# Performance work log

Hardware: AMD Instinct MI355X
Metric: run time of the kernel (lower is better)

Reference implementation:

```python
import jax, jax.numpy as jnp
import numpy as np

DIM = 64; N_C = 2000; N_P = 1500; N_ATOMS = 40; L_PROT = 512
N_FP = 10000; N_WORD = 8000; DIM_D = 1024; DIM_P = 1024
L_GNN = 3; L_CNN = 3; L_GCN = 2; WIN = 5; B = 4096


def setup_inputs() -> dict:
    key = jax.random.key(0)
    ks = jax.random.split(key, 32)
    g = lambda i, shape, s=0.05: jax.random.normal(ks[i], shape, dtype=jnp.float32) * s
    inp = {}
    inp["idx_c"] = jax.random.randint(ks[0], (B,), 0, N_C)
    inp["idx_p"] = jax.random.randint(ks[1], (B,), 0, N_P)
    inp["compounds"] = jax.random.randint(ks[2], (N_C, N_ATOMS), 0, N_FP)
    inp["proteins"] = jax.random.randint(ks[3], (N_P, L_PROT), 0, N_WORD)
    a = (jax.random.uniform(ks[4], (N_C, N_ATOMS, N_ATOMS)) < 0.1).astype(jnp.float32)
    inp["adjacencies"] = jnp.clip(a + jnp.swapaxes(a, 1, 2) + jnp.eye(N_ATOMS), 0.0, 1.0)
    ac = (jax.random.uniform(ks[5], (N_C, N_C)) < 0.005).astype(jnp.float32)
    inp["A_c"] = jnp.clip(ac + ac.T + jnp.eye(N_C), 0.0, 1.0) / 20.0
    ap = (jax.random.uniform(ks[6], (N_P, N_P)) < 0.005).astype(jnp.float32)
    inp["A_p"] = jnp.clip(ap + ap.T + jnp.eye(N_P), 0.0, 1.0) / 20.0
    inp["embed_fp"] = g(7, (N_FP, DIM), 1.0)
    inp["embed_word"] = g(8, (N_WORD, DIM), 1.0)
    inp["Xs_c"] = g(9, (N_C, DIM), 1.0)
    inp["Xs_p"] = g(10, (N_P, DIM), 1.0)
    inp["drug_feat"] = g(11, (N_C, DIM_D), 1.0)
    inp["protein_feat"] = g(12, (N_P, DIM_P), 1.0)
    inp["W_gnn"] = g(13, (L_GNN, DIM, DIM)); inp["b_gnn"] = jnp.zeros((L_GNN, DIM), jnp.float32)
    inp["K_cnn"] = g(14, (L_CNN, 2 * WIN + 1, 2 * WIN + 1)); inp["b_cnn"] = jnp.zeros((L_CNN,), jnp.float32)
    inp["W_gcn_d"] = g(15, (L_GCN, DIM, DIM)); inp["b_gcn_d"] = jnp.zeros((L_GCN, DIM), jnp.float32)
    inp["W_gcn_p"] = g(16, (L_GCN, DIM, DIM)); inp["b_gcn_p"] = jnp.zeros((L_GCN, DIM), jnp.float32)
    inp["Wd1"] = g(17, (DIM_D, 2 * DIM)); inp["bd1"] = jnp.zeros((2 * DIM,), jnp.float32)
    inp["Wd2"] = g(18, (2 * DIM, DIM)); inp["bd2"] = jnp.zeros((DIM,), jnp.float32)
    inp["Wd3"] = g(19, (DIM, DIM)); inp["bd3"] = jnp.zeros((DIM,), jnp.float32)
    inp["Wp1"] = g(20, (DIM_P, 2 * DIM)); inp["bp1"] = jnp.zeros((2 * DIM,), jnp.float32)
    inp["Wp2"] = g(21, (2 * DIM, DIM)); inp["bp2"] = jnp.zeros((DIM,), jnp.float32)
    inp["Wp3"] = g(22, (DIM, DIM)); inp["bp3"] = jnp.zeros((DIM,), jnp.float32)
    inp["Wo1"] = g(23, (6 * DIM, 4 * DIM)); inp["bo1"] = jnp.zeros((4 * DIM,), jnp.float32)
    inp["Wo2"] = g(24, (4 * DIM, 4 * DIM)); inp["bo2"] = jnp.zeros((4 * DIM,), jnp.float32)
    inp["Wo3"] = g(25, (4 * DIM, 4 * DIM)); inp["bo3"] = jnp.zeros((4 * DIM,), jnp.float32)
    inp["W_int"] = g(26, (4 * DIM, 2)); inp["b_int"] = jnp.zeros((2,), jnp.float32)
    return inp


def reference(idx_c, idx_p, compounds, proteins, adjacencies, A_c, A_p,
              embed_fp, embed_word, Xs_c, Xs_p, drug_feat, protein_feat,
              W_gnn, b_gnn, K_cnn, b_cnn, W_gcn_d, b_gcn_d, W_gcn_p, b_gcn_p,
              Wd1, bd1, Wd2, bd2, Wd3, bd3, Wp1, bp1, Wp2, bp2, Wp3, bp3,
              Wo1, bo1, Wo2, bo2, Wo3, bo3, W_int, b_int):
    # ---- intrinsic compound embedding: batched GNN over all compounds.
    # (travInvolve's BFS selects a superset of idx_c; computing all rows is
    #  output-equivalent since only Xs_c_int[idx_c] is consumed.)
    xs = embed_fp[compounds]                                  # [N_c, A, d]
    for i in range(L_GNN):
        hs = jax.nn.relu(jnp.einsum('nad,de->nae', xs, W_gnn[i]) + b_gnn[i])
        xs = xs + jnp.einsum('nab,nbd->nad', adjacencies, hs)
    comp_int = jnp.mean(xs, axis=1)                           # [N_c, d]

    # ---- intrinsic protein embedding: batched single-channel 2D CNN (SAME pad)
    x = embed_word[proteins][:, None]                         # [N_p, 1, L, d]
    for i in range(L_CNN):
        x = jax.nn.relu(jax.lax.conv_general_dilated(
            x, K_cnn[i][None, None], (1, 1), [(WIN, WIN), (WIN, WIN)]) + b_cnn[i])
    prot_int = jnp.mean(x[:, 0], axis=1)                      # mean over length -> [N_p, d]

    # ---- relational GCN diffusion over global adjacency
    Xc = Xs_c
    for i in range(L_GCN):
        Xc = jax.nn.relu((A_c @ Xc) @ W_gcn_d[i] + b_gcn_d[i])
    Xp = Xs_p
    for i in range(L_GCN):
        Xp = jax.nn.relu((A_p @ Xp) @ W_gcn_p[i] + b_gcn_p[i])

    # ---- annotation MLPs
    fd = jax.nn.relu(drug_feat[idx_c] @ Wd1 + bd1)
    fd = jax.nn.relu(fd @ Wd2 + bd2)
    fd = jax.nn.relu(fd @ Wd3 + bd3)
    fp = jax.nn.relu(protein_feat[idx_p] @ Wp1 + bp1)
    fp = jax.nn.relu(fp @ Wp2 + bp2)
    fp = jax.nn.relu(fp @ Wp3 + bp3)

    cat = jnp.concatenate([comp_int[idx_c], Xc[idx_c], fd,
                           prot_int[idx_p], Xp[idx_p], fp], axis=1)  # [B, 6d]
    h = jax.nn.relu(cat @ Wo1 + bo1)
    h = jax.nn.relu(h @ Wo2 + bo2)
    h = jax.nn.relu(h @ Wo3 + bo3)
    return jax.nn.sigmoid(h @ W_int + b_int)                  # [B, 2]
```

## Files before the change

### kernel.cpp

```cpp
#include <hip/hip_runtime.h>
#include <math.h>

#define NC 2000
#define NP 1500
#define NA 40
#define LP 512
#define BSZ 4096
#define NW 8000
#define KPC 2048
#define KPP 1536

typedef _Float16 half8_t __attribute__((ext_vector_type(8)));
typedef _Float16 half4_t __attribute__((ext_vector_type(4)));
typedef float f32x4 __attribute__((ext_vector_type(4)));

__device__ __forceinline__ int swz_off(int row, int half_col)
{
    int b = half_col >> 3;
    return row * 128 + (((b & 8) | ((b ^ row) & 7)) << 3) + (half_col & 7);
}

__global__ void prep_all(
    const float* __restrict__ K_cnn, _Float16* __restrict__ wtab,
    const float* __restrict__ ew, _Float16* __restrict__ ehp,
    const float* __restrict__ df, const float* __restrict__ pf,
    const float* __restrict__ wd1, const float* __restrict__ wd2, const float* __restrict__ wd3,
    const float* __restrict__ wp1, const float* __restrict__ wp2, const float* __restrict__ wp3,
    const float* __restrict__ wo1, const float* __restrict__ wo2, const float* __restrict__ wo3,
    _Float16* __restrict__ dfh, _Float16* __restrict__ pfh,
    _Float16* __restrict__ wd1t, _Float16* __restrict__ wd2t, _Float16* __restrict__ wd3t,
    _Float16* __restrict__ wp1t, _Float16* __restrict__ wp2t, _Float16* __restrict__ wp3t,
    _Float16* __restrict__ wo1t, _Float16* __restrict__ wo2t, _Float16* __restrict__ wo3t,
    const float* __restrict__ wgnn, _Float16* __restrict__ wgt,
    const float* __restrict__ Ac, const float* __restrict__ Ap,
    const float* __restrict__ Xc, const float* __restrict__ Xp,
    _Float16* __restrict__ Ahc, _Float16* __restrict__ Ahp,
    _Float16* __restrict__ Xtc, _Float16* __restrict__ Xtp,
    _Float16* __restrict__ Xtca, _Float16* __restrict__ Xtpa)
{
    int j = blockIdx.x * 256 + threadIdx.x;
    if (j < 16896) {
        int L = j / 5632, rem = j % 5632;
        int dr = rem >> 9, r2 = rem & 511, ln = r2 >> 3, i = r2 & 7;
        int dc = 8 * (ln >> 4) + i - (ln & 15);
        float v = (dc >= 0 && dc < 11) ? K_cnn[L * 121 + dr * 11 + dc] : 0.f;
        wtab[j] = (_Float16)v;
        return;
    }
    j -= 16896;
    if (j < NW * 80) {
        int w = j / 80, h = j - w * 80;
        float v = (h >= 13 && h < 77) ? ew[w * 64 + (h - 13)] : 0.f;
        ehp[j] = (_Float16)v;
        return;
    }
    j -= NW * 80;
    if (j < 2048000) { dfh[j] = (_Float16)df[j]; return; }
    j -= 2048000;
    if (j < 1536000) { pfh[j] = (_Float16)pf[j]; return; }
    j -= 1536000;
    if (j < 131072) { int n = j >> 10, k = j & 1023; wd1t[j] = (_Float16)wd1[k * 128 + n]; return; }
    j -= 131072;
    if (j < 8192)  { int n = j >> 7, k = j & 127; wd2t[j] = (_Float16)wd2[k * 64 + n]; return; }
    j -= 8192;
    if (j < 4096)  { int n = j >> 6, k = j & 63; wd3t[j] = (_Float16)wd3[k * 64 + n]; return; }
    j -= 4096;
    if (j < 131072) { int n = j >> 10, k = j & 1023; wp1t[j] = (_Float16)wp1[k * 128 + n]; return; }
    j -= 131072;
    if (j < 8192)  { int n = j >> 7, k = j & 127; wp2t[j] = (_Float16)wp2[k * 64 + n]; return; }
    j -= 8192;
    if (j < 4096)  { int n = j >> 6, k = j & 63; wp3t[j] = (_Float16)wp3[k * 64 + n]; return; }
    j -= 4096;
    if (j < 98304) { int n = j / 384, k = j - n * 384; wo1t[j] = (_Float16)wo1[k * 256 + n]; return; }
    j -= 98304;
    if (j < 65536) { int n = j >> 8, k = j & 255; wo2t[j] = (_Float16)wo2[k * 256 + n]; return; }
    j -= 65536;
    if (j < 65536) { int n = j >> 8, k = j & 255; wo3t[j] = (_Float16)wo3[k * 256 + n]; return; }
    j -= 65536;
    if (j < 12288) { int l = j >> 12, rem = j & 4095, nn = rem >> 6, k = rem & 63;
                     wgt[j] = (_Float16)wgnn[l * 4096 + k * 64 + nn]; return; }
    j -= 12288;
    if (j < KPC * KPC) {
        int r = j >> 11, c = j & (KPC - 1);
        Ahc[j] = (_Float16)((r < NC && c < NC) ? Ac[(size_t)r * NC + c] : 0.f);
        return;
    }
    j -= KPC * KPC;
    if (j < KPP * KPP) {
        int r = j / KPP, c = j - r * KPP;
        Ahp[j] = (_Float16)((r < NP && c < NP) ? Ap[(size_t)r * NP + c] : 0.f);
        return;
    }
    j -= KPP * KPP;
    if (j < 64 * KPC) {
        int c = j >> 11, r = j & (KPC - 1);
        Xtc[j] = (_Float16)((r < NC) ? Xc[(size_t)r * 64 + c] : 0.f);
        return;
    }
    j -= 64 * KPC;
    if (j < 64 * KPP) {
        int c = j / KPP, r = j - c * KPP;
        Xtp[j] = (_Float16)((r < NP) ? Xp[(size_t)r * 64 + c] : 0.f);
        return;
    }
    j -= 64 * KPP;
    if (j < 64 * KPC) { Xtca[j] = (_Float16)0.f; return; }
    j -= 64 * KPC;
    if (j < 64 * KPP) { Xtpa[j] = (_Float16)0.f; }
}
#define PREP_TOTAL (16896 + NW * 80 + 2048000 + 1536000 + 131072 + 8192 + 4096 + 131072 + 8192 + 4096 + 98304 + 65536 + 65536 + 12288 + KPC * KPC + KPP * KPP + 64 * KPC + 64 * KPP + 64 * KPC + 64 * KPP)

__global__ __launch_bounds__(256) void mega_kernel(
    const int* __restrict__ proteins, const _Float16* __restrict__ ehp,
    const half8_t* __restrict__ wtab, const float* __restrict__ b_cnn,
    float* __restrict__ prot_part,
    const int* __restrict__ compounds, const float* __restrict__ adjacencies,
    const float* __restrict__ embed_fp, const _Float16* __restrict__ wgt,
    const float* __restrict__ b_gnn, _Float16* __restrict__ comp_h)
{
    __shared__ union SM {
        struct { half8_t bufA8[62 * 16]; half8_t bufB8[62 * 16]; } c;
        struct { _Float16 xs[48 * 72]; _Float16 hsT[64 * 72]; } g;
    } sm;
    const int bx = blockIdx.x;
    const int tid = threadIdx.x;
    const int lane = tid & 63, wid = tid >> 6;
    const int m = lane & 15, g = lane >> 4;

    if (bx < NC) {
        auto& G = sm.g;
        const int n = bx;
        const int colL = wid * 16 + m;

        for (int j = tid; j < 48 * 64; j += 256) {
            int r = j >> 6, c = j & 63;
            _Float16 v = (_Float16)0.f;
            if (r < 40) v = (_Float16)embed_fp[(size_t)compounds[n * NA + r] * 64 + c];
            G.xs[r * 72 + c] = v;
        }
        for (int j = tid; j < 64 * 72 / 8; j += 256) ((half8_t*)G.hsT)[j] = (half8_t){};

        half8_t adjf[3][2];
        #pragma unroll
        for (int t = 0; t < 3; ++t)
            #pragma unroll
            for (int s = 0; s < 2; ++s) {
                half8_t v = {};
                int row = t * 16 + m, k0 = s * 32 + 8 * g;
                if (row < 40 && k0 < 40) {
                    const float* src = &adjacencies[(size_t)n * 1600 + row * 40 + k0];
                    #pragma unroll
                    for (int i = 0; i < 8; ++i) v[i] = (_Float16)src[i];
                }
                adjf[t][s] = v;
            }
        __syncthreads();

        for (int l = 0; l < 3; ++l) {
            float bcol = b_gnn[l * 64 + colL];
            #pragma unroll
            for (int t = 0; t < 3; ++t) {
                f32x4 acc = {bcol, bcol, bcol, bcol};
                #pragma unroll
                for (int s = 0; s < 2; ++s) {
                    half8_t a = *(const half8_t*)&G.xs[(t * 16 + m) * 72 + s * 32 + 8 * g];
                    half8_t b = *(const half8_t*)&wgt[(size_t)(l * 64 + colL) * 64 + s * 32 + 8 * g];
                    acc = __builtin_amdgcn_mfma_f32_16x16x32_f16(a, b, acc, 0, 0, 0);
                }
                half4_t h4;
                #pragma unroll
                for (int j = 0; j < 4; ++j) h4[j] = (_Float16)fmaxf(acc[j], 0.f);
                *(half4_t*)&G.hsT[colL * 72 + t * 16 + 4 * g] = h4;
            }
            __syncthreads();
            #pragma unroll
            for (int t = 0; t < 3; ++t) {
                f32x4 acc;
                #pragma unroll
                for (int j = 0; j < 4; ++j)
                    acc[j] = (float)G.xs[(t * 16 + 4 * g + j) * 72 + colL];
                #pragma unroll
                for (int s = 0; s < 2; ++s) {
                    half8_t b = *(const half8_t*)&G.hsT[colL * 72 + s * 32 + 8 * g];
                    acc = __builtin_amdgcn_mfma_f32_16x16x32_f16(adjf[t][s], b, acc, 0, 0, 0);
                }
                #pragma unroll
                for (int j = 0; j < 4; ++j)
                    G.xs[(t * 16 + 4 * g + j) * 72 + colL] = (_Float16)acc[j];
            }
            __syncthreads();
        }
        if (tid < 64) {
            float s = 0.f;
            for (int r = 0; r < 40; ++r) s += (float)G.xs[r * 72 + tid];
            comp_h[n * 64 + tid] = (_Float16)(s * (1.0f / 40.0f));
        }
        return;
    }

    _Float16* bufA = (_Float16*)sm.c.bufA8;
    _Float16* bufB = (_Float16*)sm.c.bufB8;
    half8_t* bufA8 = sm.c.bufA8;
    half8_t* bufB8 = sm.c.bufB8;

    const int cb_ = bx - NC;
    const int tile = cb_ & 15, p = cb_ >> 4;
    const int t0 = tile * 32;
    const int c0 = wid * 16;

    half8_t z = {};
    for (int e = tid; e < 62 * 9; e += 256) {
        int i = e / 9, a = 1 + (e - 9 * i);
        int gr = t0 - 15 + i;
        half8_t v = z;
        if (gr >= 0 && gr < LP)
            v = *(const half8_t*)&ehp[(size_t)proteins[p * LP + gr] * 80 + 8 * a];
        *(half8_t*)&bufA[i * 128 + (((a & 8) | ((a ^ i) & 7)) << 3)] = v;
    }
    for (int e = tid; e < 62 * 4; e += 256) {
        int i = e >> 2, w = e & 3;
        if (w == 0)      bufA8[i * 16 + (8 | ((10 ^ i) & 7))] = z;
        else if (w == 1) bufB8[i * 16 + ((1 ^ i) & 7)] = z;
        else {
            int blk = 7 + w;
            bufB8[i * 16 + ((blk & 8) | ((blk ^ i) & 7))] = z;
        }
    }

    half8_t wf[11];
    auto load_wf = [&](int L) {
        #pragma unroll
        for (int dr = 0; dr < 11; ++dr) wf[dr] = wtab[L * 11 * 64 + dr * 64 + lane];
    };
    auto conv_tile = [&](const _Float16* src, int r0, float bias) -> f32x4 {
        f32x4 acc = {bias, bias, bias, bias};
        const int B0 = (c0 + 8) >> 3;
        #pragma unroll
        for (int dr = 0; dr < 11; ++dr) {
            int R = r0 - 5 + dr + m;
            int b = B0 + g;
            half8_t a = *(const half8_t*)&src[R * 128 + (((b & 8) | ((b ^ R) & 7)) << 3)];
            acc = __builtin_amdgcn_mfma_f32_16x16x32_f16(a, wf[dr], acc, 0, 0, 0);
        }
        return acc;
    };
    auto store_tile = [&](_Float16* dst, int r0, f32x4 acc) {
        int pc = c0 + 13 + m;
        #pragma unroll
        for (int j = 0; j < 4; ++j) {
            int row = r0 + 4 * g + j;
            int og = t0 - 15 + row;
            float v = fmaxf(acc[j], 0.f);
            dst[swz_off(row, pc)] = (_Float16)((og >= 0 && og < LP) ? v : 0.f);
        }
    };

    load_wf(0);
    __syncthreads();
    {
        float b0 = b_cnn[0];
        const int r0s[4] = {5, 21, 37, 41};
        #pragma unroll
        for (int k = 0; k < 4; ++k) store_tile(bufB, r0s[k], conv_tile(bufA, r0s[k], b0));
    }
    __syncthreads();
    load_wf(1);
    {
        float b1 = b_cnn[1];
        const int r0s[3] = {10, 26, 36};
        #pragma unroll
        for (int k = 0; k < 3; ++k) store_tile(bufA, r0s[k], conv_tile(bufB, r0s[k], b1));
    }
    __syncthreads();
    load_wf(2);
    {
        float b2 = b_cnn[2];
        float cs = 0.f;
        const int r0s[2] = {15, 31};
        #pragma unroll
        for (int k = 0; k < 2; ++k) {
            f32x4 acc = conv_tile(bufA, r0s[k], b2);
            #pragma unroll
            for (int j = 0; j < 4; ++j) cs += fmaxf(acc[j], 0.f);
        }
        cs += __shfl_xor(cs, 16, 64);
        cs += __shfl_xor(cs, 32, 64);
        if (lane < 16)
            prot_part[((size_t)p * 16 + tile) * 64 + c0 + lane] = cs;
    }
}

__global__ void cnn_reduce(const float* __restrict__ prot_part, _Float16* __restrict__ prot_h)
{
    const int p = blockIdx.x, c = threadIdx.x;
    float s = 0.f;
    for (int t = 0; t < 16; ++t) s += prot_part[((size_t)p * 16 + t) * 64 + c];
    prot_h[p * 64 + c] = (_Float16)(s * (1.0f / 512.0f));
}

__global__ __launch_bounds__(256) void spk_mfma_dual(
    const _Float16* __restrict__ Ah0, const _Float16* __restrict__ Xt0, float* __restrict__ P0, int M0, int Kp0,
    const _Float16* __restrict__ Ah1, const _Float16* __restrict__ Xt1, float* __restrict__ P1, int M1, int Kp1,
    int nx1)
{
    const _Float16* Ah; const _Float16* Xt; float* part; int M, Kp;
    if (blockIdx.z == 0) { Ah = Ah0; Xt = Xt0; part = P0; M = M0; Kp = Kp0; }
    else { if ((int)blockIdx.x >= nx1) return; Ah = Ah1; Xt = Xt1; part = P1; M = M1; Kp = Kp1; }

    const int tid = threadIdx.x, wid = tid >> 6, lane = tid & 63;
    const int m = lane & 15, g = lane >> 4;
    const int row0 = blockIdx.x * 64 + wid * 16;
    const int chunk = Kp >> 3, k0 = blockIdx.y * chunk;
    const _Float16* Apr = Ah + (size_t)(row0 + m) * Kp + 8 * g;
    f32x4 acc[4] = {};
    for (int kb = k0; kb < k0 + chunk; kb += 32) {
        half8_t af = *(const half8_t*)&Apr[kb];
        #pragma unroll
        for (int t = 0; t < 4; ++t) {
            half8_t bf = *(const half8_t*)&Xt[(size_t)(t * 16 + m) * Kp + kb + 8 * g];
            acc[t] = __builtin_amdgcn_mfma_f32_16x16x32_f16(af, bf, acc[t], 0, 0, 0);
        }
    }
    const int s = blockIdx.y;
    #pragma unroll
    for (int t = 0; t < 4; ++t)
        #pragma unroll
        for (int j = 0; j < 4; ++j) {
            int row = row0 + 4 * g + j;
            if (row < M) part[((size_t)s * M + row) * 64 + t * 16 + m] = acc[t][j];
        }
}

__global__ __launch_bounds__(256) void gcn_epi_dual(
    const float* __restrict__ P0, int M0, const float* __restrict__ W0, const float* __restrict__ b0,
    _Float16* __restrict__ H0, _Float16* __restrict__ XtN0, int Kp0,
    const float* __restrict__ P1, int M1, const float* __restrict__ W1, const float* __restrict__ b1,
    _Float16* __restrict__ H1, _Float16* __restrict__ XtN1, int Kp1, int nx1)
{
    const float* part; const float* W; const float* bias; _Float16* H; _Float16* XtN; int M, Kp;
    if (blockIdx.z == 0) { part = P0; W = W0; bias = b0; H = H0; XtN = XtN0; M = M0; Kp = Kp0; }
    else { if ((int)blockIdx.x >= nx1) return; part = P1; W = W1; bias = b1; H = H1; XtN = XtN1; M = M1; Kp = Kp1; }

    __shared__ float Ys[64][68];
    __shared__ float Ws[64][64];
    const int rb = blockIdx.x * 64;
    const int tid = threadIdx.x;
    for (int j = tid; j < 4096; j += 256) Ws[j >> 6][j & 63] = W[j];
    for (int j = tid; j < 4096; j += 256) {
        int r = j >> 6, c = j & 63;
        float sum = 0.f;
        if (rb + r < M)
            for (int t = 0; t < 8; ++t) sum += part[((size_t)t * M + rb + r) * 64 + c];
        Ys[r][c] = sum;
    }
    __syncthreads();
    const int tx = tid & 15, ty = tid >> 4;
    float acc[4][4];
    #pragma unroll
    for (int i = 0; i < 4; ++i)
        #pragma unroll
        for (int j = 0; j < 4; ++j) acc[i][j] = bias[tx * 4 + j];
    for (int d = 0; d < 64; ++d) {
        float a0 = Ys[ty * 4 + 0][d], a1 = Ys[ty * 4 + 1][d];
        float a2 = Ys[ty * 4 + 2][d], a3 = Ys[ty * 4 + 3][d];
        float4 w4 = *(const float4*)&Ws[d][tx * 4];
        acc[0][0] += a0 * w4.x; acc[0][1] += a0 * w4.y; acc[0][2] += a0 * w4.z; acc[0][3] += a0 * w4.w;
        acc[1][0] += a1 * w4.x; acc[1][1] += a1 * w4.y; acc[1][2] += a1 * w4.z; acc[1][3] += a1 * w4.w;
        acc[2][0] += a2 * w4.x; acc[2][1] += a2 * w4.y; acc[2][2] += a2 * w4.z; acc[2][3] += a2 * w4.w;
        acc[3][0] += a3 * w4.x; acc[3][1] += a3 * w4.y; acc[3][2] += a3 * w4.z; acc[3][3] += a3 * w4.w;
    }
    #pragma unroll
    for (int i = 0; i < 4; ++i) {
        int row = rb + ty * 4 + i;
        if (row < M) {
            #pragma unroll
            for (int j = 0; j < 4; ++j) {
                int col = tx * 4 + j;
                float v = fmaxf(acc[i][j], 0.f);
                if (H)   H[(size_t)row * 64 + col] = (_Float16)v;
                if (XtN) XtN[(size_t)col * Kp + row] = (_Float16)v;
            }
        }
    }
}

template<int NT, bool GATHER>
__global__ __launch_bounds__(256) void mfma_mlp(
    const _Float16* __restrict__ A0, const int* __restrict__ idx0,
    const _Float16* __restrict__ Bt0, const float* __restrict__ bias0, _Float16* __restrict__ C0,
    const _Float16* __restrict__ A1, const int* __restrict__ idx1,
    const _Float16* __restrict__ Bt1, const float* __restrict__ bias1, _Float16* __restrict__ C1,
    int K, int N)
{
    const _Float16* A; const int* idx; const _Float16* Bt; const float* bias; _Float16* C;
    if (blockIdx.z == 0) { A = A0; idx = idx0; Bt = Bt0; bias = bias0; C = C0; }
    else                 { A = A1; idx = idx1; Bt = Bt1; bias = bias1; C = C1; }
    const int tid = threadIdx.x, wid = tid >> 6, lane = tid & 63;
    const int m = lane & 15, g = lane >> 4;
    const int row0 = blockIdx.x * 64 + wid * 16;
    const int col0 = blockIdx.y * (NT * 16);
    size_t arow = GATHER ? (size_t)idx[row0 + m] : (size_t)(row0 + m);
    const _Float16* Ap = A + arow * (size_t)K + 8 * g;
    f32x4 acc[NT] = {};
    for (int kb = 0; kb < K; kb += 32) {
        half8_t af = *(const half8_t*)&Ap[kb];
        #pragma unroll
        for (int t = 0; t < NT; ++t) {
            half8_t bf = *(const half8_t*)&Bt[(size_t)(col0 + t * 16 + m) * K + kb + 8 * g];
            acc[t] = __builtin_amdgcn_mfma_f32_16x16x32_f16(af, bf, acc[t], 0, 0, 0);
        }
    }
    __shared__ float cb[4][16][17];
    const int rr = lane >> 2, c4 = (lane & 3) * 4;
    #pragma unroll
    for (int t = 0; t < NT; ++t) {
        #pragma unroll
        for (int j = 0; j < 4; ++j) cb[wid][4 * g + j][m] = acc[t][j];
        half4_t h;
        #pragma unroll
        for (int j = 0; j < 4; ++j)
            h[j] = (_Float16)fmaxf(cb[wid][rr][c4 + j] + bias[col0 + t * 16 + c4 + j], 0.f);
        *(half4_t*)&C[(size_t)(row0 + rr) * N + col0 + t * 16 + c4] = h;
    }
}

__global__ __launch_bounds__(256) void mfma_head1(
    const int* __restrict__ idx_c, const int* __restrict__ idx_p,
    const _Float16* __restrict__ ci, const _Float16* __restrict__ xc, const _Float16* __restrict__ fd,
    const _Float16* __restrict__ pi, const _Float16* __restrict__ xp, const _Float16* __restrict__ fp,
    const _Float16* __restrict__ Bt, const float* __restrict__ bias, _Float16* __restrict__ C)
{
    const int tid = threadIdx.x, wid = tid >> 6, lane = tid & 63;
    const int m = lane & 15, g = lane >> 4;
    const int row0 = blockIdx.x * 64 + wid * 16;
    const int col0 = blockIdx.y * 32;
    int ic = idx_c[row0 + m], ip = idx_p[row0 + m];
    const _Float16* segs[6] = {
        ci + (size_t)ic * 64 + 8 * g,  xc + (size_t)ic * 64 + 8 * g,
        fd + (size_t)(row0 + m) * 64 + 8 * g,
        pi + (size_t)ip * 64 + 8 * g,  xp + (size_t)ip * 64 + 8 * g,
        fp + (size_t)(row0 + m) * 64 + 8 * g };
    f32x4 acc[2] = {};
    #pragma unroll
    for (int kb = 0; kb < 384; kb += 32) {
        half8_t af = *(const half8_t*)&segs[kb / 64][kb & 63];
        #pragma unroll
        for (int t = 0; t < 2; ++t) {
            half8_t bf = *(const half8_t*)&Bt[(size_t)(col0 + t * 16 + m) * 384 + kb + 8 * g];
            acc[t] = __builtin_amdgcn_mfma_f32_16x16x32_f16(af, bf, acc[t], 0, 0, 0);
        }
    }
    __shared__ float cb[4][16][17];
    const int rr = lane >> 2, c4 = (lane & 3) * 4;
    #pragma unroll
    for (int t = 0; t < 2; ++t) {
        #pragma unroll
        for (int j = 0; j < 4; ++j) cb[wid][4 * g + j][m] = acc[t][j];
        half4_t h;
        #pragma unroll
        for (int j = 0; j < 4; ++j)
            h[j] = (_Float16)fmaxf(cb[wid][rr][c4 + j] + bias[col0 + t * 16 + c4 + j], 0.f);
        *(half4_t*)&C[(size_t)(row0 + rr) * 256 + col0 + t * 16 + c4] = h;
    }
}

__global__ __launch_bounds__(256) void mfma_head3(
    const _Float16* __restrict__ A, const _Float16* __restrict__ Bt,
    const float* __restrict__ bias, const float* __restrict__ Wi, const float* __restrict__ bi,
    float* __restrict__ out)
{
    const int tid = threadIdx.x, wid = tid >> 6, lane = tid & 63;
    const int m = lane & 15, g = lane >> 4;
    const int row0 = blockIdx.x * 64 + wid * 16;
    const _Float16* Ap = A + (size_t)(row0 + m) * 256 + 8 * g;
    f32x4 acc[16] = {};
    for (int kb = 0; kb < 256; kb += 32) {
        half8_t af = *(const half8_t*)&Ap[kb];
        #pragma unroll
        for (int t = 0; t < 16; ++t) {
            half8_t bf = *(const half8_t*)&Bt[(size_t)(t * 16 + m) * 256 + kb + 8 * g];
            acc[t] = __builtin_amdgcn_mfma_f32_16x16x32_f16(af, bf, acc[t], 0, 0, 0);
        }
    }
    float p0[4] = {}, p1[4] = {};
    #pragma unroll
    for (int t = 0; t < 16; ++t) {
        float w0 = Wi[(t * 16 + m) * 2], w1 = Wi[(t * 16 + m) * 2 + 1];
        float bc = bias[t * 16 + m];
        #pragma unroll
        for (int j = 0; j < 4; ++j) {
            float v = fmaxf(acc[t][j] + bc, 0.f);
            p0[j] += v * w0; p1[j] += v * w1;
        }
    }
    #pragma unroll
    for (int d = 1; d < 16; d <<= 1) {
        #pragma unroll
        for (int j = 0; j < 4; ++j) {
            p0[j] += __shfl_xor(p0[j], d, 64);
            p1[j] += __shfl_xor(p1[j], d, 64);
        }
    }
    if (m == 0) {
        float B0 = bi[0], B1 = bi[1];
        #pragma unroll
        for (int j = 0; j < 4; ++j) {
            int r = row0 + 4 * g + j;
            out[r * 2 + 0] = 1.f / (1.f + expf(-(p0[j] + B0)));
            out[r * 2 + 1] = 1.f / (1.f + expf(-(p1[j] + B1)));
        }
    }
}

extern "C" void kernel_launch(void* const* d_in, const int* in_sizes, int n_in,
                              void* d_out, int out_size, void* d_ws, size_t ws_size,
                              hipStream_t stream)
{
    const int*   idx_c        = (const int*)  d_in[0];
    const int*   idx_p        = (const int*)  d_in[1];
    const int*   compounds    = (const int*)  d_in[2];
    const int*   proteins     = (const int*)  d_in[3];
    const float* adjacencies  = (const float*)d_in[4];
    const float* A_c          = (const float*)d_in[5];
    const float* A_p          = (const float*)d_in[6];
    const float* embed_fp     = (const float*)d_in[7];
    const float* embed_word   = (const float*)d_in[8];
    const float* Xs_c         = (const float*)d_in[9];
    const float* Xs_p         = (const float*)d_in[10];
    const float* drug_feat    = (const float*)d_in[11];
    const float* protein_feat = (const float*)d_in[12];
    const float* W_gnn        = (const float*)d_in[13];
    const float* b_gnn        = (const float*)d_in[14];
    const float* K_cnn        = (const float*)d_in[15];
    const float* b_cnn        = (const float*)d_in[16];
    const float* W_gcn_d      = (const float*)d_in[17];
    const float* b_gcn_d      = (const float*)d_in[18];
    const float* W_gcn_p      = (const float*)d_in[19];
    const float* b_gcn_p      = (const float*)d_in[20];
    const float* Wd1 = (const float*)d_in[21]; const float* bd1 = (const float*)d_in[22];
    const float* Wd2 = (const float*)d_in[23]; const float* bd2 = (const float*)d_in[24];
    const float* Wd3 = (const float*)d_in[25]; const float* bd3 = (const float*)d_in[26];
    const float* Wp1 = (const float*)d_in[27]; const float* bp1 = (const float*)d_in[28];
    const float* Wp2 = (const float*)d_in[29]; const float* bp2 = (const float*)d_in[30];
    const float* Wp3 = (const float*)d_in[31]; const float* bp3 = (const float*)d_in[32];
    const float* Wo1 = (const float*)d_in[33]; const float* bo1 = (const float*)d_in[34];
    const float* Wo2 = (const float*)d_in[35]; const float* bo2 = (const float*)d_in[36];
    const float* Wo3 = (const float*)d_in[37]; const float* bo3 = (const float*)d_in[38];
    const float* W_int = (const float*)d_in[39]; const float* b_int = (const float*)d_in[40];

    float* ws = (float*)d_ws;
    float* prot_part = ws; ws += NP * 16 * 64;
    float* wtab_g    = ws; ws += 8448;
    float* ehp_g     = ws; ws += NW * 40;
    float* part_c    = ws; ws += 8 * NC * 64;
    float* part_p    = ws; ws += 8 * NP * 64;
    _Float16* Ah_c  = (_Float16*)ws; ws += KPC * KPC / 2;
    _Float16* Ah_p  = (_Float16*)ws; ws += KPP * KPP / 2;
    _Float16* Xt_c  = (_Float16*)ws; ws += 32 * KPC;
    _Float16* Xt_p  = (_Float16*)ws; ws += 32 * KPP;
    _Float16* Xt_ca = (_Float16*)ws; ws += 32 * KPC;
    _Float16* Xt_pa = (_Float16*)ws; ws += 32 * KPP;
    _Float16* wgt_g = (_Float16*)ws; ws += 6144;
    _Float16* comp_h  = (_Float16*)ws; ws += NC * 32;
    _Float16* prot_h  = (_Float16*)ws; ws += NP * 32;
    _Float16* Xcb_h   = (_Float16*)ws; ws += NC * 32;
    _Float16* Xpb_h   = (_Float16*)ws; ws += NP * 32;
    _Float16* drug_h  = (_Float16*)ws; ws += NC * 512;
    _Float16* protf_h = (_Float16*)ws; ws += NP * 512;
    _Float16* wd1t = (_Float16*)ws; ws += 65536;
    _Float16* wd2t = (_Float16*)ws; ws += 4096;
    _Float16* wd3t = (_Float16*)ws; ws += 2048;
    _Float16* wp1t = (_Float16*)ws; ws += 65536;
    _Float16* wp2t = (_Float16*)ws; ws += 4096;
    _Float16* wp3t = (_Float16*)ws; ws += 2048;
    _Float16* wo1t = (_Float16*)ws; ws += 49152;
    _Float16* wo2t = (_Float16*)ws; ws += 32768;
    _Float16* wo3t = (_Float16*)ws; ws += 32768;
    _Float16* fd1h = (_Float16*)ws; ws += BSZ * 64;
    _Float16* fd2h = (_Float16*)ws; ws += BSZ * 32;
    _Float16* fd3h = (_Float16*)ws; ws += BSZ * 32;
    _Float16* fp1h = (_Float16*)ws; ws += BSZ * 64;
    _Float16* fp2h = (_Float16*)ws; ws += BSZ * 32;
    _Float16* fp3h = (_Float16*)ws; ws += BSZ * 32;
    _Float16* h1h  = (_Float16*)ws; ws += BSZ * 128;
    _Float16* h2h  = (_Float16*)ws; ws += BSZ * 128;
    (void)ws_size; (void)in_sizes; (void)n_in; (void)out_size;

    prep_all<<<(PREP_TOTAL + 255) / 256, 256, 0, stream>>>(
        K_cnn, (_Float16*)wtab_g, embed_word, (_Float16*)ehp_g,
        drug_feat, protein_feat, Wd1, Wd2, Wd3, Wp1, Wp2, Wp3, Wo1, Wo2, Wo3,
        drug_h, protf_h, wd1t, wd2t, wd3t, wp1t, wp2t, wp3t, wo1t, wo2t, wo3t,
        W_gnn, wgt_g,
        A_c, A_p, Xs_c, Xs_p, Ah_c, Ah_p, Xt_c, Xt_p, Xt_ca, Xt_pa);
    mega_kernel<<<NC + 16 * NP, 256, 0, stream>>>(
        proteins, (const _Float16*)ehp_g, (const half8_t*)wtab_g, b_cnn, prot_part,
        compounds, adjacencies, embed_fp, wgt_g, b_gnn, comp_h);
    cnn_reduce<<<NP, 64, 0, stream>>>(prot_part, prot_h);
    spk_mfma_dual<<<dim3(32, 8, 2), 256, 0, stream>>>(
        Ah_c, Xt_c, part_c, NC, KPC, Ah_p, Xt_p, part_p, NP, KPP, 24);
    gcn_epi_dual<<<dim3(32, 1, 2), 256, 0, stream>>>(
        part_c, NC, W_gcn_d, b_gcn_d, nullptr, Xt_ca, KPC,
        part_p, NP, W_gcn_p, b_gcn_p, nullptr, Xt_pa, KPP, 24);
    spk_mfma_dual<<<dim3(32, 8, 2), 256, 0, stream>>>(
        Ah_c, Xt_ca, part_c, NC, KPC, Ah_p, Xt_pa, part_p, NP, KPP, 24);
    gcn_epi_dual<<<dim3(32, 1, 2), 256, 0, stream>>>(
        part_c, NC, W_gcn_d + 4096, b_gcn_d + 64, Xcb_h, nullptr, KPC,
        part_p, NP, W_gcn_p + 4096, b_gcn_p + 64, Xpb_h, nullptr, KPP, 24);
    mfma_mlp<2, true ><<<dim3(64, 4, 2), 256, 0, stream>>>(
        drug_h, idx_c, wd1t, bd1, fd1h, protf_h, idx_p, wp1t, bp1, fp1h, 1024, 128);
    mfma_mlp<1, false><<<dim3(64, 4, 2), 256, 0, stream>>>(
        fd1h, nullptr, wd2t, bd2, fd2h, fp1h, nullptr, wp2t, bp2, fp2h, 128, 64);
    mfma_mlp<1, false><<<dim3(64, 4, 2), 256, 0, stream>>>(
        fd2h, nullptr, wd3t, bd3, fd3h, fp2h, nullptr, wp3t, bp3, fp3h, 64, 64);
    mfma_head1<<<dim3(64, 8), 256, 0, stream>>>(idx_c, idx_p, comp_h, Xcb_h, fd3h,
                                                prot_h, Xpb_h, fp3h, wo1t, bo1, h1h);
    mfma_mlp<2, false><<<dim3(64, 8, 1), 256, 0, stream>>>(
        h1h, nullptr, wo2t, bo2, h2h, h1h, nullptr, wo2t, bo2, h2h, 256, 256);
    mfma_head3<<<64, 256, 0, stream>>>(h2h, wo3t, bo3, W_int, b_int, (float*)d_out);
}
```

Before: 349.0 us.

## Merge independent stages into shared kernels to cut launch count

```diff
diff --git a/kernel.cpp b/kernel.cpp
--- a/kernel.cpp
+++ b/kernel.cpp
@@ -13,6 +13,11 @@
 typedef _Float16 half8_t __attribute__((ext_vector_type(8)));
 typedef _Float16 half4_t __attribute__((ext_vector_type(4)));
 typedef float f32x4 __attribute__((ext_vector_type(4)));
+
+struct CnnS { half8_t bufA8[62 * 16]; half8_t bufB8[62 * 16]; };
+struct GnnS { _Float16 xs[48 * 72]; _Float16 hsT[64 * 72]; };
+struct MlpS { float cb[4][16][17]; };
+struct EpiS { float Ys[64][68]; float Ws[64][64]; };
 
 __device__ __forceinline__ int swz_off(int row, int half_col)
 {
@@ -110,103 +115,94 @@
 }
 #define PREP_TOTAL (16896 + NW * 80 + 2048000 + 1536000 + 131072 + 8192 + 4096 + 131072 + 8192 + 4096 + 98304 + 65536 + 65536 + 12288 + KPC * KPC + KPP * KPP + 64 * KPC + 64 * KPP + 64 * KPC + 64 * KPP)
 
-__global__ __launch_bounds__(256) void mega_kernel(
-    const int* __restrict__ proteins, const _Float16* __restrict__ ehp,
-    const half8_t* __restrict__ wtab, const float* __restrict__ b_cnn,
-    float* __restrict__ prot_part,
+__device__ __forceinline__ void gnn_body(GnnS& G, int n,
     const int* __restrict__ compounds, const float* __restrict__ adjacencies,
     const float* __restrict__ embed_fp, const _Float16* __restrict__ wgt,
     const float* __restrict__ b_gnn, _Float16* __restrict__ comp_h)
 {
-    __shared__ union SM {
-        struct { half8_t bufA8[62 * 16]; half8_t bufB8[62 * 16]; } c;
-        struct { _Float16 xs[48 * 72]; _Float16 hsT[64 * 72]; } g;
-    } sm;
-    const int bx = blockIdx.x;
-    const int tid = threadIdx.x;
-    const int lane = tid & 63, wid = tid >> 6;
+    const int tid = threadIdx.x, lane = tid & 63, wid = tid >> 6;
     const int m = lane & 15, g = lane >> 4;
-
-    if (bx < NC) {
-        auto& G = sm.g;
-        const int n = bx;
-        const int colL = wid * 16 + m;
-
-        for (int j = tid; j < 48 * 64; j += 256) {
-            int r = j >> 6, c = j & 63;
-            _Float16 v = (_Float16)0.f;
-            if (r < 40) v = (_Float16)embed_fp[(size_t)compounds[n * NA + r] * 64 + c];
-            G.xs[r * 72 + c] = v;
-        }
-        for (int j = tid; j < 64 * 72 / 8; j += 256) ((half8_t*)G.hsT)[j] = (half8_t){};
-
-        half8_t adjf[3][2];
-        #pragma unroll
-        for (int t = 0; t < 3; ++t)
+    const int colL = wid * 16 + m;
+
+    for (int j = tid; j < 48 * 64; j += 256) {
+        int r = j >> 6, c = j & 63;
+        _Float16 v = (_Float16)0.f;
+        if (r < 40) v = (_Float16)embed_fp[(size_t)compounds[n * NA + r] * 64 + c];
+        G.xs[r * 72 + c] = v;
+    }
+    for (int j = tid; j < 64 * 72 / 8; j += 256) ((half8_t*)G.hsT)[j] = (half8_t){};
+
+    half8_t adjf[3][2];
+    #pragma unroll
+    for (int t = 0; t < 3; ++t)
+        #pragma unroll
+        for (int s = 0; s < 2; ++s) {
+            half8_t v = {};
+            int row = t * 16 + m, k0 = s * 32 + 8 * g;
+            if (row < 40 && k0 < 40) {
+                const float* src = &adjacencies[(size_t)n * 1600 + row * 40 + k0];
+                #pragma unroll
+                for (int i = 0; i < 8; ++i) v[i] = (_Float16)src[i];
+            }
+            adjf[t][s] = v;
+        }
+    __syncthreads();
+
+    for (int l = 0; l < 3; ++l) {
+        float bcol = b_gnn[l * 64 + colL];
+        #pragma unroll
+        for (int t = 0; t < 3; ++t) {
+            f32x4 acc = {bcol, bcol, bcol, bcol};
             #pragma unroll
             for (int s = 0; s < 2; ++s) {
-                half8_t v = {};
-                int row = t * 16 + m, k0 = s * 32 + 8 * g;
-                if (row < 40 && k0 < 40) {
-                    const float* src = &adjacencies[(size_t)n * 1600 + row * 40 + k0];
-                    #pragma unroll
-                    for (int i = 0; i < 8; ++i) v[i] = (_Float16)src[i];
-                }
-                adjf[t][s] = v;
+                half8_t a = *(const half8_t*)&G.xs[(t * 16 + m) * 72 + s * 32 + 8 * g];
+                half8_t b = *(const half8_t*)&wgt[(size_t)(l * 64 + colL) * 64 + s * 32 + 8 * g];
+                acc = __builtin_amdgcn_mfma_f32_16x16x32_f16(a, b, acc, 0, 0, 0);
             }
+            half4_t h4;
+            #pragma unroll
+            for (int j = 0; j < 4; ++j) h4[j] = (_Float16)fmaxf(acc[j], 0.f);
+            *(half4_t*)&G.hsT[colL * 72 + t * 16 + 4 * g] = h4;
+        }
         __syncthreads();
-
-        for (int l = 0; l < 3; ++l) {
-            float bcol = b_gnn[l * 64 + colL];
+        #pragma unroll
+        for (int t = 0; t < 3; ++t) {
+            f32x4 acc;
             #pragma unroll
-            for (int t = 0; t < 3; ++t) {
-                f32x4 acc = {bcol, bcol, bcol, bcol};
-                #pragma unroll
-                for (int s = 0; s < 2; ++s) {
-                    half8_t a = *(const half8_t*)&G.xs[(t * 16 + m) * 72 + s * 32 + 8 * g];
-                    half8_t b = *(const half8_t*)&wgt[(size_t)(l * 64 + colL) * 64 + s * 32 + 8 * g];
-                    acc = __builtin_amdgcn_mfma_f32_16x16x32_f16(a, b, acc, 0, 0, 0);
-                }
-                half4_t h4;
-                #pragma unroll
-                for (int j = 0; j < 4; ++j) h4[j] = (_Float16)fmaxf(acc[j], 0.f);
-                *(half4_t*)&G.hsT[colL * 72 + t * 16 + 4 * g] = h4;
+            for (int j = 0; j < 4; ++j)
+                acc[j] = (float)G.xs[(t * 16 + 4 * g + j) * 72 + colL];
+            #pragma unroll
+            for (int s = 0; s < 2; ++s) {
+                half8_t b = *(const half8_t*)&G.hsT[colL * 72 + s * 32 + 8 * g];
+                acc = __builtin_amdgcn_mfma_f32_16x16x32_f16(adjf[t][s], b, acc, 0, 0, 0);
             }
-            __syncthreads();
             #pragma unroll
-            for (int t = 0; t < 3; ++t) {
-                f32x4 acc;
-                #pragma unroll
-                for (int j = 0; j < 4; ++j)
-                    acc[j] = (float)G.xs[(t * 16 + 4 * g + j) * 72 + colL];
-                #pragma unroll
-                for (int s = 0; s < 2; ++s) {
-                    half8_t b = *(const half8_t*)&G.hsT[colL * 72 + s * 32 + 8 * g];
-                    acc = __builtin_amdgcn_mfma_f32_16x16x32_f16(adjf[t][s], b, acc, 0, 0, 0);
-                }
-                #pragma unroll
-                for (int j = 0; j < 4; ++j)
-                    G.xs[(t * 16 + 4 * g + j) * 72 + colL] = (_Float16)acc[j];
-            }
-            __syncthreads();
-        }
-        if (tid < 64) {
-            float s = 0.f;
-            for (int r = 0; r < 40; ++r) s += (float)G.xs[r * 72 + tid];
-            comp_h[n * 64 + tid] = (_Float16)(s * (1.0f / 40.0f));
-        }
-        return;
-    }
-
-    _Float16* bufA = (_Float16*)sm.c.bufA8;
-    _Float16* bufB = (_Float16*)sm.c.bufB8;
-    half8_t* bufA8 = sm.c.bufA8;
-    half8_t* bufB8 = sm.c.bufB8;
-
-    const int cb_ = bx - NC;
+            for (int j = 0; j < 4; ++j)
+                G.xs[(t * 16 + 4 * g + j) * 72 + colL] = (_Float16)acc[j];
+        }
+        __syncthreads();
+    }
+    if (tid < 64) {
+        float s = 0.f;
+        for (int r = 0; r < 40; ++r) s += (float)G.xs[r * 72 + tid];
+        comp_h[n * 64 + tid] = (_Float16)(s * (1.0f / 40.0f));
+    }
+}
+
+__device__ __forceinline__ void cnn_body(CnnS& S, int cb_,
+    const int* __restrict__ proteins, const _Float16* __restrict__ ehp,
+    const half8_t* __restrict__ wtab, const float* __restrict__ b_cnn,
+    float* __restrict__ prot_part)
+{
+    _Float16* bufA = (_Float16*)S.bufA8;
+    _Float16* bufB = (_Float16*)S.bufB8;
+    half8_t* bufA8 = S.bufA8;
+    half8_t* bufB8 = S.bufB8;
+    const int tid = threadIdx.x, lane = tid & 63, wid = tid >> 6;
     const int tile = cb_ & 15, p = cb_ >> 4;
     const int t0 = tile * 32;
     const int c0 = wid * 16;
+    const int m = lane & 15, g = lane >> 4;
 
     half8_t z = {};
     for (int e = tid; e < 62 * 9; e += 256) {
@@ -290,27 +286,14 @@
     }
 }
 
-__global__ void cnn_reduce(const float* __restrict__ prot_part, _Float16* __restrict__ prot_h)
-{
-    const int p = blockIdx.x, c = threadIdx.x;
-    float s = 0.f;
-    for (int t = 0; t < 16; ++t) s += prot_part[((size_t)p * 16 + t) * 64 + c];
-    prot_h[p * 64 + c] = (_Float16)(s * (1.0f / 512.0f));
-}
-
-__global__ __launch_bounds__(256) void spk_mfma_dual(
-    const _Float16* __restrict__ Ah0, const _Float16* __restrict__ Xt0, float* __restrict__ P0, int M0, int Kp0,
-    const _Float16* __restrict__ Ah1, const _Float16* __restrict__ Xt1, float* __restrict__ P1, int M1, int Kp1,
-    int nx1)
-{
-    const _Float16* Ah; const _Float16* Xt; float* part; int M, Kp;
-    if (blockIdx.z == 0) { Ah = Ah0; Xt = Xt0; part = P0; M = M0; Kp = Kp0; }
-    else { if ((int)blockIdx.x >= nx1) return; Ah = Ah1; Xt = Xt1; part = P1; M = M1; Kp = Kp1; }
-
+__device__ __forceinline__ void spk_body(int x, int y,
+    const _Float16* __restrict__ Ah, const _Float16* __restrict__ Xt,
+    float* __restrict__ part, int M, int Kp)
+{
     const int tid = threadIdx.x, wid = tid >> 6, lane = tid & 63;
     const int m = lane & 15, g = lane >> 4;
-    const int row0 = blockIdx.x * 64 + wid * 16;
-    const int chunk = Kp >> 3, k0 = blockIdx.y * chunk;
+    const int row0 = x * 64 + wid * 16;
+    const int chunk = Kp >> 3, k0 = y * chunk;
     const _Float16* Apr = Ah + (size_t)(row0 + m) * Kp + 8 * g;
     f32x4 acc[4] = {};
     for (int kb = k0; kb < k0 + chunk; kb += 32) {
@@ -321,37 +304,29 @@
             acc[t] = __builtin_amdgcn_mfma_f32_16x16x32_f16(af, bf, acc[t], 0, 0, 0);
         }
     }
-    const int s = blockIdx.y;
     #pragma unroll
     for (int t = 0; t < 4; ++t)
         #pragma unroll
         for (int j = 0; j < 4; ++j) {
             int row = row0 + 4 * g + j;
-            if (row < M) part[((size_t)s * M + row) * 64 + t * 16 + m] = acc[t][j];
-        }
-}
-
-__global__ __launch_bounds__(256) void gcn_epi_dual(
-    const float* __restrict__ P0, int M0, const float* __restrict__ W0, const float* __restrict__ b0,
-    _Float16* __restrict__ H0, _Float16* __restrict__ XtN0, int Kp0,
-    const float* __restrict__ P1, int M1, const float* __restrict__ W1, const float* __restrict__ b1,
-    _Float16* __restrict__ H1, _Float16* __restrict__ XtN1, int Kp1, int nx1)
-{
-    const float* part; const float* W; const float* bias; _Float16* H; _Float16* XtN; int M, Kp;
-    if (blockIdx.z == 0) { part = P0; W = W0; bias = b0; H = H0; XtN = XtN0; M = M0; Kp = Kp0; }
-    else { if ((int)blockIdx.x >= nx1) return; part = P1; W = W1; bias = b1; H = H1; XtN = XtN1; M = M1; Kp = Kp1; }
-
-    __shared__ float Ys[64][68];
-    __shared__ float Ws[64][64];
-    const int rb = blockIdx.x * 64;
+            if (row < M) part[((size_t)y * M + row) * 64 + t * 16 + m] = acc[t][j];
+        }
+}
+
+__device__ __forceinline__ void epi_body(EpiS& S, int x,
+    const float* __restrict__ part, int M, const float* __restrict__ W,
+    const float* __restrict__ bias, _Float16* __restrict__ H,
+    _Float16* __restrict__ XtN, int Kp)
+{
+    const int rb = x * 64;
     const int tid = threadIdx.x;
-    for (int j = tid; j < 4096; j += 256) Ws[j >> 6][j & 63] = W[j];
+    for (int j = tid; j < 4096; j += 256) S.Ws[j >> 6][j & 63] = W[j];
     for (int j = tid; j < 4096; j += 256) {
         int r = j >> 6, c = j & 63;
         float sum = 0.f;
         if (rb + r < M)
             for (int t = 0; t < 8; ++t) sum += part[((size_t)t * M + rb + r) * 64 + c];
-        Ys[r][c] = sum;
+        S.Ys[r][c] = sum;
     }
     __syncthreads();
     const int tx = tid & 15, ty = tid >> 4;
@@ -361,9 +336,9 @@
         #pragma unroll
         for (int j = 0; j < 4; ++j) acc[i][j] = bias[tx * 4 + j];
     for (int d = 0; d < 64; ++d) {
-        float a0 = Ys[ty * 4 + 0][d], a1 = Ys[ty * 4 + 1][d];
-        float a2 = Ys[ty * 4 + 2][d], a3 = Ys[ty * 4 + 3][d];
-        float4 w4 = *(const float4*)&Ws[d][tx * 4];
+        float a0 = S.Ys[ty * 4 + 0][d], a1 = S.Ys[ty * 4 + 1][d];
+        float a2 = S.Ys[ty * 4 + 2][d], a3 = S.Ys[ty * 4 + 3][d];
+        float4 w4 = *(const float4*)&S.Ws[d][tx * 4];
         acc[0][0] += a0 * w4.x; acc[0][1] += a0 * w4.y; acc[0][2] += a0 * w4.z; acc[0][3] += a0 * w4.w;
         acc[1][0] += a1 * w4.x; acc[1][1] += a1 * w4.y; acc[1][2] += a1 * w4.z; acc[1][3] += a1 * w4.w;
         acc[2][0] += a2 * w4.x; acc[2][1] += a2 * w4.y; acc[2][2] += a2 * w4.z; acc[2][3] += a2 * w4.w;
@@ -385,20 +360,15 @@
 }
 
 template<int NT, bool GATHER>
-__global__ __launch_bounds__(256) void mfma_mlp(
-    const _Float16* __restrict__ A0, const int* __restrict__ idx0,
-    const _Float16* __restrict__ Bt0, const float* __restrict__ bias0, _Float16* __restrict__ C0,
-    const _Float16* __restrict__ A1, const int* __restrict__ idx1,
-    const _Float16* __restrict__ Bt1, const float* __restrict__ bias1, _Float16* __restrict__ C1,
-    int K, int N)
-{
-    const _Float16* A; const int* idx; const _Float16* Bt; const float* bias; _Float16* C;
-    if (blockIdx.z == 0) { A = A0; idx = idx0; Bt = Bt0; bias = bias0; C = C0; }
-    else                 { A = A1; idx = idx1; Bt = Bt1; bias = bias1; C = C1; }
+__device__ __forceinline__ void mlp_body(MlpS& S, int x, int y,
+    const _Float16* __restrict__ A, const int* __restrict__ idx,
+    const _Float16* __restrict__ Bt, const float* __restrict__ bias,
+    _Float16* __restrict__ C, int K, int N)
+{
     const int tid = threadIdx.x, wid = tid >> 6, lane = tid & 63;
     const int m = lane & 15, g = lane >> 4;
-    const int row0 = blockIdx.x * 64 + wid * 16;
-    const int col0 = blockIdx.y * (NT * 16);
+    const int row0 = x * 64 + wid * 16;
+    const int col0 = y * (NT * 16);
     size_t arow = GATHER ? (size_t)idx[row0 + m] : (size_t)(row0 + m);
     const _Float16* Ap = A + arow * (size_t)K + 8 * g;
     f32x4 acc[NT] = {};
@@ -410,18 +380,133 @@
             acc[t] = __builtin_amdgcn_mfma_f32_16x16x32_f16(af, bf, acc[t], 0, 0, 0);
         }
     }
-    __shared__ float cb[4][16][17];
     const int rr = lane >> 2, c4 = (lane & 3) * 4;
     #pragma unroll
     for (int t = 0; t < NT; ++t) {
         #pragma unroll
-        for (int j = 0; j < 4; ++j) cb[wid][4 * g + j][m] = acc[t][j];
+        for (int j = 0; j < 4; ++j) S.cb[wid][4 * g + j][m] = acc[t][j];
         half4_t h;
         #pragma unroll
         for (int j = 0; j < 4; ++j)
-            h[j] = (_Float16)fmaxf(cb[wid][rr][c4 + j] + bias[col0 + t * 16 + c4 + j], 0.f);
+            h[j] = (_Float16)fmaxf(S.cb[wid][rr][c4 + j] + bias[col0 + t * 16 + c4 + j], 0.f);
         *(half4_t*)&C[(size_t)(row0 + rr) * N + col0 + t * 16 + c4] = h;
     }
+}
+
+#define MEGA_CNN0 NC
+#define MEGA_SPK0 (NC + 16 * NP)
+#define MEGA_MLP0 (MEGA_SPK0 + 512)
+#define MEGA_TOTAL (MEGA_MLP0 + 512)
+
+__global__ __launch_bounds__(256) void mega_kernel(
+    const int* __restrict__ proteins, const _Float16* __restrict__ ehp,
+    const half8_t* __restrict__ wtab, const float* __restrict__ b_cnn,
+    float* __restrict__ prot_part,
+    const int* __restrict__ compounds, const float* __restrict__ adjacencies,
+    const float* __restrict__ embed_fp, const _Float16* __restrict__ wgt,
+    const float* __restrict__ b_gnn, _Float16* __restrict__ comp_h,
+    const _Float16* __restrict__ Ah_c, const _Float16* __restrict__ Xt_c, float* __restrict__ part_c,
+    const _Float16* __restrict__ Ah_p, const _Float16* __restrict__ Xt_p, float* __restrict__ part_p,
+    const _Float16* __restrict__ drug_h, const int* __restrict__ idx_c,
+    const _Float16* __restrict__ wd1t, const float* __restrict__ bd1, _Float16* __restrict__ fd1h,
+    const _Float16* __restrict__ protf_h, const int* __restrict__ idx_p,
+    const _Float16* __restrict__ wp1t, const float* __restrict__ bp1, _Float16* __restrict__ fp1h)
+{
+    __shared__ union { CnnS c; GnnS g; MlpS m; } sm;
+    const int bx = blockIdx.x;
+
+    if (bx >= MEGA_MLP0) {
+        int idx = bx - MEGA_MLP0;
+        int z = idx >> 8, rem = idx & 255, y = rem >> 6, x = rem & 63;
+        if (z == 0) mlp_body<2, true>(sm.m, x, y, drug_h, idx_c, wd1t, bd1, fd1h, 1024, 128);
+        else        mlp_body<2, true>(sm.m, x, y, protf_h, idx_p, wp1t, bp1, fp1h, 1024, 128);
+        return;
+    }
+    if (bx >= MEGA_SPK0) {
+        int idx = bx - MEGA_SPK0;
+        int z = idx >> 8, rem = idx & 255, y = rem >> 5, x = rem & 31;
+        if (z == 0)      spk_body(x, y, Ah_c, Xt_c, part_c, NC, KPC);
+        else if (x < 24) spk_body(x, y, Ah_p, Xt_p, part_p, NP, KPP);
+        return;
+    }
+    if (bx < MEGA_CNN0) {
+        gnn_body(sm.g, bx, compounds, adjacencies, embed_fp, wgt, b_gnn, comp_h);
+        return;
+    }
+    cnn_body(sm.c, bx - MEGA_CNN0, proteins, ehp, wtab, b_cnn, prot_part);
+}
+
+__global__ __launch_bounds__(256) void tail1(
+    const float* __restrict__ prot_part, _Float16* __restrict__ prot_h,
+    const float* __restrict__ part_c, const float* __restrict__ W_gcn_d, const float* __restrict__ b_gcn_d,
+    _Float16* __restrict__ Xt_ca,
+    const float* __restrict__ part_p, const float* __restrict__ W_gcn_p, const float* __restrict__ b_gcn_p,
+    _Float16* __restrict__ Xt_pa,
+    const _Float16* __restrict__ fd1h, const _Float16* __restrict__ wd2t, const float* __restrict__ bd2,
+    _Float16* __restrict__ fd2h,
+    const _Float16* __restrict__ fp1h, const _Float16* __restrict__ wp2t, const float* __restrict__ bp2,
+    _Float16* __restrict__ fp2h)
+{
+    __shared__ union { EpiS e; MlpS m; } sm;
+    int bx = blockIdx.x;
+    const int tid = threadIdx.x;
+    if (bx < 375) {
+        int p = bx * 4 + (tid >> 6), c = tid & 63;
+        float s = 0.f;
+        for (int t = 0; t < 16; ++t) s += prot_part[((size_t)p * 16 + t) * 64 + c];
+        prot_h[p * 64 + c] = (_Float16)(s * (1.0f / 512.0f));
+        return;
+    }
+    bx -= 375;
+    if (bx < 64) {
+        int z = bx >> 5, x = bx & 31;
+        if (z == 0)      epi_body(sm.e, x, part_c, NC, W_gcn_d, b_gcn_d, nullptr, Xt_ca, KPC);
+        else if (x < 24) epi_body(sm.e, x, part_p, NP, W_gcn_p, b_gcn_p, nullptr, Xt_pa, KPP);
+        return;
+    }
+    bx -= 64;
+    {
+        int z = bx >> 8, rem = bx & 255, y = rem >> 6, x = rem & 63;
+        if (z == 0) mlp_body<1, false>(sm.m, x, y, fd1h, nullptr, wd2t, bd2, fd2h, 128, 64);
+        else        mlp_body<1, false>(sm.m, x, y, fp1h, nullptr, wp2t, bp2, fp2h, 128, 64);
+    }
+}
+
+__global__ __launch_bounds__(256) void tail2(
+    const _Float16* __restrict__ Ah_c, const _Float16* __restrict__ Xt_ca, float* __restrict__ part_c,
+    const _Float16* __restrict__ Ah_p, const _Float16* __restrict__ Xt_pa, float* __restrict__ part_p,
+    const _Float16* __restrict__ fd2h, const _Float16* __restrict__ wd3t, const float* __restrict__ bd3,
+    _Float16* __restrict__ fd3h,
+    const _Float16* __restrict__ fp2h, const _Float16* __restrict__ wp3t, const float* __restrict__ bp3,
+    _Float16* __restrict__ fp3h)
+{
+    __shared__ MlpS sm;
+    int bx = blockIdx.x;
+    if (bx < 512) {
+        int z = bx >> 8, rem = bx & 255, y = rem >> 5, x = rem & 31;
+        if (z == 0)      spk_body(x, y, Ah_c, Xt_ca, part_c, NC, KPC);
+        else if (x < 24) spk_body(x, y, Ah_p, Xt_pa, part_p, NP, KPP);
+        return;
+    }
+    bx -= 512;
+    {
+        int z = bx >> 8, rem = bx & 255, y = rem >> 6, x = rem & 63;
+        if (z == 0) mlp_body<1, false>(sm, x, y, fd2h, nullptr, wd3t, bd3, fd3h, 64, 64);
+        else        mlp_body<1, false>(sm, x, y, fp2h, nullptr, wp3t, bp3, fp3h, 64, 64);
+    }
+}
+
+__global__ __launch_bounds__(256) void epi2_kernel(
+    const float* __restrict__ part_c, const float* __restrict__ W0, const float* __restrict__ b0,
+    _Float16* __restrict__ Xcb_h,
+    const float* __restrict__ part_p, const float* __restrict__ W1, const float* __restrict__ b1,
+    _Float16* __restrict__ Xpb_h)
+{
+    __shared__ EpiS sm;
+    int bx = blockIdx.x;
+    int z = bx >> 5, x = bx & 31;
+    if (z == 0)      epi_body(sm, x, part_c, NC, W0, b0, Xcb_h, nullptr, KPC);
+    else if (x < 24) epi_body(sm, x, part_p, NP, W1, b1, Xpb_h, nullptr, KPP);
 }
 
 __global__ __launch_bounds__(256) void mfma_head1(
@@ -450,18 +535,26 @@
             acc[t] = __builtin_amdgcn_mfma_f32_16x16x32_f16(af, bf, acc[t], 0, 0, 0);
         }
     }
-    __shared__ float cb[4][16][17];
+    __shared__ MlpS sm;
     const int rr = lane >> 2, c4 = (lane & 3) * 4;
     #pragma unroll
     for (int t = 0; t < 2; ++t) {
         #pragma unroll
-        for (int j = 0; j < 4; ++j) cb[wid][4 * g + j][m] = acc[t][j];
+        for (int j = 0; j < 4; ++j) sm.cb[wid][4 * g + j][m] = acc[t][j];
         half4_t h;
         #pragma unroll
         for (int j = 0; j < 4; ++j)
-            h[j] = (_Float16)fmaxf(cb[wid][rr][c4 + j] + bias[col0 + t * 16 + c4 + j], 0.f);
+            h[j] = (_Float16)fmaxf(sm.cb[wid][rr][c4 + j] + bias[col0 + t * 16 + c4 + j], 0.f);
         *(half4_t*)&C[(size_t)(row0 + rr) * 256 + col0 + t * 16 + c4] = h;
     }
+}
+
+__global__ __launch_bounds__(256) void mfma_head2(
+    const _Float16* __restrict__ A, const _Float16* __restrict__ Bt,
+    const float* __restrict__ bias, _Float16* __restrict__ C)
+{
+    __shared__ MlpS sm;
+    mlp_body<2, false>(sm, blockIdx.x, blockIdx.y, A, nullptr, Bt, bias, C, 256, 256);
 }
 
 __global__ __launch_bounds__(256) void mfma_head3(
@@ -592,29 +685,23 @@
         drug_h, protf_h, wd1t, wd2t, wd3t, wp1t, wp2t, wp3t, wo1t, wo2t, wo3t,
         W_gnn, wgt_g,
         A_c, A_p, Xs_c, Xs_p, Ah_c, Ah_p, Xt_c, Xt_p, Xt_ca, Xt_pa);
-    mega_kernel<<<NC + 16 * NP, 256, 0, stream>>>(
+    mega_kernel<<<MEGA_TOTAL, 256, 0, stream>>>(
         proteins, (const _Float16*)ehp_g, (const half8_t*)wtab_g, b_cnn, prot_part,
-        compounds, adjacencies, embed_fp, wgt_g, b_gnn, comp_h);
-    cnn_reduce<<<NP, 64, 0, stream>>>(prot_part, prot_h);
-    spk_mfma_dual<<<dim3(32, 8, 2), 256, 0, stream>>>(
-        Ah_c, Xt_c, part_c, NC, KPC, Ah_p, Xt_p, part_p, NP, KPP, 24);
-    gcn_epi_dual<<<dim3(32, 1, 2), 256, 0, stream>>>(
-        part_c, NC, W_gcn_d, b_gcn_d, nullptr, Xt_ca, KPC,
-        part_p, NP, W_gcn_p, b_gcn_p, nullptr, Xt_pa, KPP, 24);
-    spk_mfma_dual<<<dim3(32, 8, 2), 256, 0, stream>>>(
-        Ah_c, Xt_ca, part_c, NC, KPC, Ah_p, Xt_pa, part_p, NP, KPP, 24);
-    gcn_epi_dual<<<dim3(32, 1, 2), 256, 0, stream>>>(
-        part_c, NC, W_gcn_d + 4096, b_gcn_d + 64, Xcb_h, nullptr, KPC,
-        part_p, NP, W_gcn_p + 4096, b_gcn_p + 64, Xpb_h, nullptr, KPP, 24);
-    mfma_mlp<2, true ><<<dim3(64, 4, 2), 256, 0, stream>>>(
-        drug_h, idx_c, wd1t, bd1, fd1h, protf_h, idx_p, wp1t, bp1, fp1h, 1024, 128);
-    mfma_mlp<1, false><<<dim3(64, 4, 2), 256, 0, stream>>>(
-        fd1h, nullptr, wd2t, bd2, fd2h, fp1h, nullptr, wp2t, bp2, fp2h, 128, 64);
-    mfma_mlp<1, false><<<dim3(64, 4, 2), 256, 0, stream>>>(
-        fd2h, nullptr, wd3t, bd3, fd3h, fp2h, nullptr, wp3t, bp3, fp3h, 64, 64);
+        compounds, adjacencies, embed_fp, wgt_g, b_gnn, comp_h,
+        Ah_c, Xt_c, part_c, Ah_p, Xt_p, part_p,
+        drug_h, idx_c, wd1t, bd1, fd1h, protf_h, idx_p, wp1t, bp1, fp1h);
+    tail1<<<375 + 64 + 512, 256, 0, stream>>>(
+        prot_part, prot_h,
+        part_c, W_gcn_d, b_gcn_d, Xt_ca, part_p, W_gcn_p, b_gcn_p, Xt_pa,
+        fd1h, wd2t, bd2, fd2h, fp1h, wp2t, bp2, fp2h);
+    tail2<<<512 + 512, 256, 0, stream>>>(
+        Ah_c, Xt_ca, part_c, Ah_p, Xt_pa, part_p,
+        fd2h, wd3t, bd3, fd3h, fp2h, wp3t, bp3, fp3h);
+    epi2_kernel<<<64, 256, 0, stream>>>(
+        part_c, W_gcn_d + 4096, b_gcn_d + 64, Xcb_h,
+        part_p, W_gcn_p + 4096, b_gcn_p + 64, Xpb_h);
     mfma_head1<<<dim3(64, 8), 256, 0, stream>>>(idx_c, idx_p, comp_h, Xcb_h, fd3h,
                                                 prot_h, Xpb_h, fp3h, wo1t, bo1, h1h);
-    mfma_mlp<2, false><<<dim3(64, 8, 1), 256, 0, stream>>>(
-        h1h, nullptr, wo2t, bo2, h2h, h1h, nullptr, wo2t, bo2, h2h, 256, 256);
+    mfma_head2<<<dim3(64, 8), 256, 0, stream>>>(h1h, wo2t, bo2, h2h);
     mfma_head3<<<64, 256, 0, stream>>>(h2h, wo3t, bo3, W_int, b_int, (float*)d_out);
 }
```

After: 365.4 us. 4.7% more time.
